# Performance work log

Hardware: AMD Instinct MI355X
Metric: run time of the kernel (lower is better)

The kernel has to match this reference:

```python
import jax, jax.numpy as jnp
import numpy as np


def setup_inputs() -> dict:
    key = jax.random.key(0)
    k1, k2, k3, k4 = jax.random.split(key, 4)
    B, Tv, Ta, D = 8, 2048, 2048, 256
    return {
        "visual_features": jax.random.normal(k1, (B, Tv, D), dtype=jnp.float32),
        "audio_features": jax.random.normal(k2, (B, Ta, D), dtype=jnp.float32),
        "visual_weights": jax.random.uniform(k3, (D, D), dtype=jnp.float32),
        "audio_weights": jax.random.uniform(k4, (D, D), dtype=jnp.float32),
        "num_neighbors": 8,
    }


def _pairwise_l2(vm, am):
    # ||v - a|| via the expanded form to avoid the [B,Tv,Ta,D] intermediate.
    sq = (
        jnp.sum(vm * vm, -1)[:, :, None]
        + jnp.sum(am * am, -1)[:, None, :]
        - 2.0 * jnp.einsum("btd,bsd->bts", vm, am)
    )
    sq = jnp.maximum(sq, 0.0)
    # safe sqrt: subgradient 0 at 0 (matches torch.norm backward convention)
    return jnp.where(sq > 0, jnp.sqrt(jnp.where(sq > 0, sq, 1.0)), 0.0)


def reference(visual_features, audio_features, visual_weights, audio_weights, num_neighbors):
    vm = visual_features @ visual_weights  # [B,Tv,D]
    am = audio_features @ audio_weights    # [B,Ta,D]
    graph = jnp.exp(-_pairwise_l2(vm, am))  # [B,Tv,Ta]
    # topk over the visual axis (dim=1): move it last for lax.top_k
    _, idx = jax.lax.top_k(jnp.swapaxes(graph, 1, 2), num_neighbors)  # [B,Ta,k]
    idx = jnp.swapaxes(idx, 1, 2)  # [B,k,Ta]
    # broadcasted gather along axis 1: result [B,k,Ta,D]
    vn = jnp.take_along_axis(visual_features[:, :, None, :], idx[..., None], axis=1)
    an = jnp.take_along_axis(audio_features[:, :, None, :], idx[..., None], axis=1)
    # mean over dim=2 (the Ta axis of the gathered neighbors) -> [B,k,D]
    return vn.mean(axis=2), an.mean(axis=2)
```

## Files before the change

### kernel.cpp

```cpp
#include <hip/hip_runtime.h>
#include <cstddef>
#include <cstdint>

namespace {
constexpr int kB   = 8;
constexpr int kT   = 2048;
constexpr int kD   = 256;
constexpr int kK   = 8;
constexpr int kM   = kB * kT;
constexpr int kNCH = 64;
constexpr int kNC  = kB * kT;
constexpr int kColCap = 64;
constexpr int kOvCap  = 1 << 17;
constexpr float kMinNormalF = 1.17549435e-38f;
}

typedef __attribute__((ext_vector_type(8)))  __bf16 bf16x8;
typedef __attribute__((ext_vector_type(16))) float  f32x16;

__device__ inline unsigned short f2bf_rne(float x) {
  unsigned u = __float_as_uint(x);
  unsigned r = (u + 0x7FFFu + ((u >> 16) & 1u)) >> 16;
  return (unsigned short)r;
}
__device__ inline float bf2f(unsigned short h) {
  return __uint_as_float((unsigned)h << 16);
}

__global__ __launch_bounds__(256) void transposeW2(const float* __restrict__ W0,
                                                   const float* __restrict__ W1,
                                                   unsigned short* __restrict__ T0,
                                                   unsigned short* __restrict__ T1) {
  const float* W = blockIdx.z ? W1 : W0;
  unsigned short* WT = blockIdx.z ? T1 : T0;
  __shared__ float tile[32][33];
  const int k0 = blockIdx.y * 32, c0 = blockIdx.x * 32;
  const int tx = threadIdx.x & 31, ty = threadIdx.x >> 5;
#pragma unroll
  for (int i = 0; i < 4; ++i)
    tile[ty + i * 8][tx] = W[(size_t)(k0 + ty + i * 8) * kD + c0 + tx];
  __syncthreads();
#pragma unroll
  for (int i = 0; i < 4; ++i)
    WT[(size_t)(c0 + ty + i * 8) * kD + k0 + tx] = f2bf_rne(tile[tx][ty + i * 8]);
}

__global__ __launch_bounds__(256) void gemm_fused(const float* __restrict__ Xv,
                                                  const float* __restrict__ Xa,
                                                  const unsigned short* __restrict__ WvT,
                                                  const unsigned short* __restrict__ WaT,
                                                  unsigned short* __restrict__ Cv,
                                                  unsigned short* __restrict__ Ca,
                                                  float* __restrict__ nv,
                                                  float* __restrict__ na) {
  __shared__ unsigned short Xs[128 * 68];
  __shared__ unsigned short Ws[64 * 68];
  const int z = blockIdx.z;
  const float* X = z ? Xa : Xv;
  const unsigned short* WT = z ? WaT : WvT;
  unsigned short* Cb = z ? Ca : Cv;
  float* nrm = z ? na : nv;
  const int r0 = blockIdx.x * 128;
  const int c0 = blockIdx.y * 64;
  const int tid = threadIdx.x;
  const int w = tid >> 6, lane = tid & 63;
  const int half = lane >> 5, ln = lane & 31;
  const int xrb = tid >> 4, xc4 = (tid & 15) * 4;
  const int wrb = tid >> 3, wc8 = (tid & 7) * 8;

  f32x16 acc[2];
#pragma unroll
  for (int j = 0; j < 2; ++j)
#pragma unroll
    for (int i = 0; i < 16; ++i) acc[j][i] = 0.0f;

  union Frag { uint2 u2[2]; bf16x8 v; };

  for (int k0 = 0; k0 < kD; k0 += 64) {
#pragma unroll
    for (int i = 0; i < 8; ++i) {
      const float4 v = *reinterpret_cast<const float4*>(X + (size_t)(r0 + i * 16 + xrb) * kD + k0 + xc4);
      ushort4 o;
      o.x = f2bf_rne(v.x); o.y = f2bf_rne(v.y); o.z = f2bf_rne(v.z); o.w = f2bf_rne(v.w);
      *reinterpret_cast<ushort4*>(Xs + (i * 16 + xrb) * 68 + xc4) = o;
    }
#pragma unroll
    for (int i = 0; i < 2; ++i) {
      const uint4 v = *reinterpret_cast<const uint4*>(WT + (size_t)(c0 + i * 32 + wrb) * kD + k0 + wc8);
      *reinterpret_cast<uint4*>(Ws + (i * 32 + wrb) * 68 + wc8) = v;
    }
    __syncthreads();
#pragma unroll
    for (int kk = 0; kk < 4; ++kk) {
      Frag fa, fb0, fb1;
      const uint2* pa = reinterpret_cast<const uint2*>(Xs + (w * 32 + ln) * 68 + kk * 16 + half * 8);
      fa.u2[0] = pa[0]; fa.u2[1] = pa[1];
      const uint2* p0 = reinterpret_cast<const uint2*>(Ws + ln * 68 + kk * 16 + half * 8);
      fb0.u2[0] = p0[0]; fb0.u2[1] = p0[1];
      const uint2* p1 = reinterpret_cast<const uint2*>(Ws + (32 + ln) * 68 + kk * 16 + half * 8);
      fb1.u2[0] = p1[0]; fb1.u2[1] = p1[1];
      acc[0] = __builtin_amdgcn_mfma_f32_32x32x16_bf16(fa.v, fb0.v, acc[0], 0, 0, 0);
      acc[1] = __builtin_amdgcn_mfma_f32_32x32x16_bf16(fa.v, fb1.v, acc[1], 0, 0, 0);
    }
    __syncthreads();
  }
  float ns[16];
#pragma unroll
  for (int r = 0; r < 16; ++r) ns[r] = 0.0f;
#pragma unroll
  for (int jj = 0; jj < 2; ++jj) {
    const int col = c0 + jj * 32 + ln;
#pragma unroll
    for (int r = 0; r < 16; ++r) {
      const int row = r0 + w * 32 + (r & 3) + 8 * (r >> 2) + 4 * half;
      const unsigned short us = f2bf_rne(acc[jj][r]);
      Cb[(size_t)row * kD + col] = us;
      const float f = bf2f(us);
      ns[r] += f * f;
    }
  }
#pragma unroll
  for (int r = 0; r < 16; ++r) {
    float v = ns[r];
#pragma unroll
    for (int off = 1; off < 32; off <<= 1) v += __shfl_xor(v, off, 64);
    if (ln == 0) {
      const int row = r0 + w * 32 + (r & 3) + 8 * (r >> 2) + 4 * half;
      atomicAdd(nrm + row, v);
    }
  }
}

__global__ __launch_bounds__(256) void keys_mfma(const unsigned short* __restrict__ vmb,
                                                 const unsigned short* __restrict__ amb,
                                                 const float* __restrict__ vn2,
                                                 const float* __restrict__ an2,
                                                 unsigned* __restrict__ colCount,
                                                 uint2* __restrict__ colRecs,
                                                 unsigned* __restrict__ ovCount,
                                                 uint2* __restrict__ ovRecs) {
  __shared__ unsigned short vmS[64 * 68];
  __shared__ unsigned short amS[64 * 68];
  const int b = blockIdx.z;
  const int t0 = blockIdx.x * 64;
  const int s0 = blockIdx.y * 64;
  const int tid = threadIdx.x;
  const int wave = tid >> 6, lane = tid & 63;
  const int wt = wave & 1, wsi = wave >> 1;
  const int half = lane >> 5, ln = lane & 31;
  const int rb = tid >> 3, c8 = (tid & 7) * 8;
  const unsigned short* vbase = vmb + ((size_t)b * kT + t0) * kD;
  const unsigned short* abase = amb + ((size_t)b * kT + s0) * kD;

  f32x16 acc;
#pragma unroll
  for (int i = 0; i < 16; ++i) acc[i] = 0.0f;

  union Frag { uint2 u2[2]; bf16x8 v; };

  for (int k0 = 0; k0 < kD; k0 += 64) {
#pragma unroll
    for (int i = 0; i < 2; ++i) {
      const int row = i * 32 + rb;
      const uint4 v = *reinterpret_cast<const uint4*>(vbase + (size_t)row * kD + k0 + c8);
      *reinterpret_cast<uint4*>(vmS + row * 68 + c8) = v;
      const uint4 a = *reinterpret_cast<const uint4*>(abase + (size_t)row * kD + k0 + c8);
      *reinterpret_cast<uint4*>(amS + row * 68 + c8) = a;
    }
    __syncthreads();
#pragma unroll
    for (int kk = 0; kk < 4; ++kk) {
      Frag fa, fb;
      const uint2* pa = reinterpret_cast<const uint2*>(vmS + (wt * 32 + ln) * 68 + kk * 16 + half * 8);
      fa.u2[0] = pa[0]; fa.u2[1] = pa[1];
      const uint2* pb = reinterpret_cast<const uint2*>(amS + (wsi * 32 + ln) * 68 + kk * 16 + half * 8);
      fb.u2[0] = pb[0]; fb.u2[1] = pb[1];
      acc = __builtin_amdgcn_mfma_f32_32x32x16_bf16(fa.v, fb.v, acc, 0, 0, 0);
    }
    __syncthreads();
  }

  const int s = s0 + wsi * 32 + ln;
  const float a2 = an2[(size_t)b * kT + s];
  const int c = (b << 11) | s;
  const float* v2p = vn2 + (size_t)b * kT + t0 + wt * 32;
#pragma unroll
  for (int g = 0; g < 4; ++g) {
    const float4 v2 = *reinterpret_cast<const float4*>(v2p + g * 8 + half * 4);
    const float v2a[4] = {v2.x, v2.y, v2.z, v2.w};
#pragma unroll
    for (int q = 0; q < 4; ++q) {
      const float dot = acc[4 * g + q];
      const float sq = fmaxf(v2a[q] + a2 - 2.0f * dot, 0.0f);
      const float dist = sqrtf(sq);
      if (dist < 88.0f) {
        const float e = expf(-dist);
        if (e >= kMinNormalF) {
          const int t = t0 + wt * 32 + g * 8 + half * 4 + q;
          const unsigned slot = atomicAdd(&colCount[c], 1u);
          if (slot < (unsigned)kColCap) {
            colRecs[(size_t)c * kColCap + slot] = make_uint2(__float_as_uint(e), (unsigned)t);
          } else {
            const unsigned pos = ((unsigned)b << 22) | ((unsigned)s << 11) | (unsigned)t;
            const unsigned oi = atomicAdd(ovCount, 1u);
            if (oi < (unsigned)kOvCap) ovRecs[oi] = make_uint2(__float_as_uint(e), pos);
          }
        }
      }
    }
  }
}

__global__ __launch_bounds__(256) void finalize_topk(const unsigned* __restrict__ colCount,
                                                     const uint2* __restrict__ colRecs,
                                                     const unsigned* __restrict__ ovCount,
                                                     const uint2* __restrict__ ovRecs,
                                                     int* __restrict__ idxT) {
  const int c = blockIdx.x * 256 + threadIdx.x;
  unsigned K[8];
  int T[8];
#pragma unroll
  for (int i = 0; i < 8; ++i) { K[i] = 0u; T[i] = 0x7FFFFFFF; }
  const int cnt = (int)colCount[c];
  const int m = min(cnt, kColCap);
  for (int i = 0; i < m; ++i) {
    const uint2 r = colRecs[(size_t)c * kColCap + i];
    const unsigned kx = r.x;
    const int tx = (int)r.y;
    if (kx > K[7] || (kx == K[7] && tx < T[7])) {
      K[7] = kx; T[7] = tx;
#pragma unroll
      for (int q = 7; q >= 1; --q) {
        const bool sw = (K[q] > K[q - 1]) || (K[q] == K[q - 1] && T[q] < T[q - 1]);
        if (sw) {
          const unsigned tk = K[q]; K[q] = K[q - 1]; K[q - 1] = tk;
          const int tt = T[q];      T[q] = T[q - 1]; T[q - 1] = tt;
        }
      }
    }
  }
  if (cnt > kColCap) {
    int n = (int)*ovCount;
    if (n > kOvCap) n = kOvCap;
    for (int i = 0; i < n; ++i) {
      const uint2 r = ovRecs[i];
      if ((int)(r.y >> 11) == c) {
        const unsigned kx = r.x;
        const int tx = (int)(r.y & 2047u);
        if (kx > K[7] || (kx == K[7] && tx < T[7])) {
          K[7] = kx; T[7] = tx;
#pragma unroll
          for (int q = 7; q >= 1; --q) {
            const bool sw = (K[q] > K[q - 1]) || (K[q] == K[q - 1] && T[q] < T[q - 1]);
            if (sw) {
              const unsigned tk = K[q]; K[q] = K[q - 1]; K[q - 1] = tk;
              const int tt = T[q];      T[q] = T[q - 1]; T[q - 1] = tt;
            }
          }
        }
      }
    }
  }
  int mcnt = 0;
#pragma unroll
  for (int i = 0; i < 8; ++i) if (K[i] > 0u) mcnt++;
  int outv[8];
#pragma unroll
  for (int i = 0; i < 8; ++i) outv[i] = T[i];
  int cand = 0;
  for (int r = mcnt; r < 8; ++r) {
    bool taken = true;
    while (taken) {
      taken = false;
#pragma unroll
      for (int q = 0; q < 8; ++q)
        if (q < mcnt && T[q] == cand) taken = true;
      if (taken) cand++;
    }
    outv[r] = cand++;
  }
  const int b = c >> 11, s = c & 2047;
#pragma unroll
  for (int r = 0; r < 8; ++r) idxT[((size_t)b * kK + r) * kT + s] = outv[r];
}

__global__ __launch_bounds__(256) void gather_kernel(const float* __restrict__ visual,
                                                     const float* __restrict__ audio,
                                                     const int* __restrict__ idxT,
                                                     float* __restrict__ pv,
                                                     float* __restrict__ pa) {
  const int blk = blockIdx.x;
  const int ch = blk & (kNCH - 1);
  const int bj = blk / kNCH;
  const int b = bj >> 3;
  const int d = threadIdx.x;
  const int* ip = idxT + (size_t)bj * kT + ch * (kT / kNCH);
  float accV = 0.f, accA = 0.f;
  for (int g = 0; g < kT / kNCH / 4; ++g) {
    const int4 cur = *reinterpret_cast<const int4*>(ip + g * 4);
    const int ts[4] = {cur.x, cur.y, cur.z, cur.w};
#pragma unroll
    for (int u = 0; u < 4; ++u) {
      const size_t base = ((size_t)b * kT + ts[u]) * kD + d;
      accV += visual[base];
      accA += audio[base];
    }
  }
  pv[(size_t)blk * kD + d] = accV;
  pa[(size_t)blk * kD + d] = accA;
}

__global__ __launch_bounds__(256) void reduce_kernel(const float* __restrict__ pv,
                                                     const float* __restrict__ pa,
                                                     float* __restrict__ out) {
  const int bj = blockIdx.x;
  const int d = threadIdx.x;
  float sV = 0.f, sA = 0.f;
#pragma unroll 8
  for (int ch = 0; ch < kNCH; ++ch) {
    sV += pv[((size_t)bj * kNCH + ch) * kD + d];
    sA += pa[((size_t)bj * kNCH + ch) * kD + d];
  }
  out[(size_t)bj * kD + d] = sV * (1.0f / kT);
  out[(size_t)kB * kK * kD + (size_t)bj * kD + d] = sA * (1.0f / kT);
}

extern "C" void kernel_launch(void* const* d_in, const int* in_sizes, int n_in,
                              void* d_out, int out_size, void* d_ws, size_t ws_size,
                              hipStream_t stream) {
  (void)in_sizes; (void)n_in; (void)out_size; (void)ws_size;
  const float* visual = (const float*)d_in[0];
  const float* audio  = (const float*)d_in[1];
  const float* Wv     = (const float*)d_in[2];
  const float* Wa     = (const float*)d_in[3];
  float* out = (float*)d_out;

  char* ws = (char*)d_ws;
  unsigned short* WvT = (unsigned short*)ws;
  unsigned short* WaT = WvT + (size_t)kD * kD;
  unsigned short* vmb = WaT + (size_t)kD * kD;
  unsigned short* amb = vmb + (size_t)kM * kD;
  float* vn2 = (float*)(amb + (size_t)kM * kD);
  float* an2 = vn2 + kM;
  unsigned* colCount = (unsigned*)(an2 + kM);
  unsigned* ovCount  = colCount + kNC;
  uint2* colRecs = (uint2*)(ovCount + 4);
  uint2* ovRecs  = colRecs + (size_t)kNC * kColCap;
  int* idxT = (int*)(ovRecs + kOvCap);
  float* pv = (float*)(idxT + (size_t)kB * kK * kT);
  float* pa = pv + (size_t)kB * kK * kNCH * kD;

  hipMemsetAsync(vn2, 0, (size_t)(2 * kM + kNC + 4) * sizeof(float), stream);
  transposeW2<<<dim3(kD / 32, kD / 32, 2), 256, 0, stream>>>(Wv, Wa, WvT, WaT);
  gemm_fused<<<dim3(kM / 128, kD / 64, 2), 256, 0, stream>>>(visual, audio, WvT, WaT,
                                                             vmb, amb, vn2, an2);
  keys_mfma<<<dim3(kT / 64, kT / 64, kB), 256, 0, stream>>>(vmb, amb, vn2, an2,
                                                            colCount, colRecs, ovCount, ovRecs);
  finalize_topk<<<dim3(kNC / 256), 256, 0, stream>>>(colCount, colRecs, ovCount, ovRecs, idxT);
  gather_kernel<<<dim3(kB * kK * kNCH), 256, 0, stream>>>(visual, audio, idxT, pv, pa);
  reduce_kernel<<<dim3(kB * kK), 256, 0, stream>>>(pv, pa, out);
}
```

Measured before the change: 175.5 us.

## Enlarge keys GEMM tile, reshape projection tile, fold reduce into gather atomics

The pairwise-distance MFMA kernel now computes a 64x128 tile per block, two MFMA accumulators per wave, so each loaded visual tile is reused across more audio columns and the block count halves. Its distance test now compares the squared distance against 7744 before taking the sqrt. The projection GEMM switches from a 128x64 to a 64x128 tile with a 2x2 wave layout. The separate reduce kernel is removed: gather blocks atomically add their scaled partial sums into a zeroed output, which saves a launch and the partial buffers but makes float summation order nondeterministic.

```diff
diff --git a/kernel.cpp b/kernel.cpp
--- a/kernel.cpp
+++ b/kernel.cpp
@@ -53,20 +53,19 @@
                                                   unsigned short* __restrict__ Ca,
                                                   float* __restrict__ nv,
                                                   float* __restrict__ na) {
-  __shared__ unsigned short Xs[128 * 68];
-  __shared__ unsigned short Ws[64 * 68];
+  __shared__ unsigned short Xs[64 * 68];
+  __shared__ unsigned short Ws[128 * 68];
   const int z = blockIdx.z;
   const float* X = z ? Xa : Xv;
   const unsigned short* WT = z ? WaT : WvT;
   unsigned short* Cb = z ? Ca : Cv;
   float* nrm = z ? na : nv;
-  const int r0 = blockIdx.x * 128;
-  const int c0 = blockIdx.y * 64;
+  const int r0 = blockIdx.x * 64;
+  const int c0 = blockIdx.y * 128;
   const int tid = threadIdx.x;
-  const int w = tid >> 6, lane = tid & 63;
+  const int wave = tid >> 6, lane = tid & 63;
+  const int wt = wave & 1, wsi = wave >> 1;
   const int half = lane >> 5, ln = lane & 31;
-  const int xrb = tid >> 4, xc4 = (tid & 15) * 4;
-  const int wrb = tid >> 3, wc8 = (tid & 7) * 8;
 
   f32x16 acc[2];
 #pragma unroll
@@ -78,26 +77,30 @@
 
   for (int k0 = 0; k0 < kD; k0 += 64) {
 #pragma unroll
-    for (int i = 0; i < 8; ++i) {
-      const float4 v = *reinterpret_cast<const float4*>(X + (size_t)(r0 + i * 16 + xrb) * kD + k0 + xc4);
+    for (int i = 0; i < 4; ++i) {
+      const int j = i * 256 + tid;
+      const int row = j >> 4, c4 = (j & 15) * 4;
+      const float4 v = *reinterpret_cast<const float4*>(X + (size_t)(r0 + row) * kD + k0 + c4);
       ushort4 o;
       o.x = f2bf_rne(v.x); o.y = f2bf_rne(v.y); o.z = f2bf_rne(v.z); o.w = f2bf_rne(v.w);
-      *reinterpret_cast<ushort4*>(Xs + (i * 16 + xrb) * 68 + xc4) = o;
-    }
-#pragma unroll
-    for (int i = 0; i < 2; ++i) {
-      const uint4 v = *reinterpret_cast<const uint4*>(WT + (size_t)(c0 + i * 32 + wrb) * kD + k0 + wc8);
-      *reinterpret_cast<uint4*>(Ws + (i * 32 + wrb) * 68 + wc8) = v;
+      *reinterpret_cast<ushort4*>(Xs + row * 68 + c4) = o;
+    }
+#pragma unroll
+    for (int i = 0; i < 4; ++i) {
+      const int j = i * 256 + tid;
+      const int row = j >> 3, c8 = (j & 7) * 8;
+      const uint4 v = *reinterpret_cast<const uint4*>(WT + (size_t)(c0 + row) * kD + k0 + c8);
+      *reinterpret_cast<uint4*>(Ws + row * 68 + c8) = v;
     }
     __syncthreads();
 #pragma unroll
     for (int kk = 0; kk < 4; ++kk) {
       Frag fa, fb0, fb1;
-      const uint2* pa = reinterpret_cast<const uint2*>(Xs + (w * 32 + ln) * 68 + kk * 16 + half * 8);
+      const uint2* pa = reinterpret_cast<const uint2*>(Xs + (wt * 32 + ln) * 68 + kk * 16 + half * 8);
       fa.u2[0] = pa[0]; fa.u2[1] = pa[1];
-      const uint2* p0 = reinterpret_cast<const uint2*>(Ws + ln * 68 + kk * 16 + half * 8);
+      const uint2* p0 = reinterpret_cast<const uint2*>(Ws + (wsi * 64 + ln) * 68 + kk * 16 + half * 8);
       fb0.u2[0] = p0[0]; fb0.u2[1] = p0[1];
-      const uint2* p1 = reinterpret_cast<const uint2*>(Ws + (32 + ln) * 68 + kk * 16 + half * 8);
+      const uint2* p1 = reinterpret_cast<const uint2*>(Ws + (wsi * 64 + 32 + ln) * 68 + kk * 16 + half * 8);
       fb1.u2[0] = p1[0]; fb1.u2[1] = p1[1];
       acc[0] = __builtin_amdgcn_mfma_f32_32x32x16_bf16(fa.v, fb0.v, acc[0], 0, 0, 0);
       acc[1] = __builtin_amdgcn_mfma_f32_32x32x16_bf16(fa.v, fb1.v, acc[1], 0, 0, 0);
@@ -109,10 +112,10 @@
   for (int r = 0; r < 16; ++r) ns[r] = 0.0f;
 #pragma unroll
   for (int jj = 0; jj < 2; ++jj) {
-    const int col = c0 + jj * 32 + ln;
+    const int col = c0 + wsi * 64 + jj * 32 + ln;
 #pragma unroll
     for (int r = 0; r < 16; ++r) {
-      const int row = r0 + w * 32 + (r & 3) + 8 * (r >> 2) + 4 * half;
+      const int row = r0 + wt * 32 + (r & 3) + 8 * (r >> 2) + 4 * half;
       const unsigned short us = f2bf_rne(acc[jj][r]);
       Cb[(size_t)row * kD + col] = us;
       const float f = bf2f(us);
@@ -125,7 +128,7 @@
 #pragma unroll
     for (int off = 1; off < 32; off <<= 1) v += __shfl_xor(v, off, 64);
     if (ln == 0) {
-      const int row = r0 + w * 32 + (r & 3) + 8 * (r >> 2) + 4 * half;
+      const int row = r0 + wt * 32 + (r & 3) + 8 * (r >> 2) + 4 * half;
       atomicAdd(nrm + row, v);
     }
   }
@@ -140,70 +143,82 @@
                                                  unsigned* __restrict__ ovCount,
                                                  uint2* __restrict__ ovRecs) {
   __shared__ unsigned short vmS[64 * 68];
-  __shared__ unsigned short amS[64 * 68];
+  __shared__ unsigned short amS[128 * 68];
   const int b = blockIdx.z;
   const int t0 = blockIdx.x * 64;
-  const int s0 = blockIdx.y * 64;
+  const int s0 = blockIdx.y * 128;
   const int tid = threadIdx.x;
   const int wave = tid >> 6, lane = tid & 63;
   const int wt = wave & 1, wsi = wave >> 1;
   const int half = lane >> 5, ln = lane & 31;
-  const int rb = tid >> 3, c8 = (tid & 7) * 8;
   const unsigned short* vbase = vmb + ((size_t)b * kT + t0) * kD;
   const unsigned short* abase = amb + ((size_t)b * kT + s0) * kD;
 
-  f32x16 acc;
-#pragma unroll
-  for (int i = 0; i < 16; ++i) acc[i] = 0.0f;
+  f32x16 acc[2];
+#pragma unroll
+  for (int j = 0; j < 2; ++j)
+#pragma unroll
+    for (int i = 0; i < 16; ++i) acc[j][i] = 0.0f;
 
   union Frag { uint2 u2[2]; bf16x8 v; };
 
   for (int k0 = 0; k0 < kD; k0 += 64) {
 #pragma unroll
     for (int i = 0; i < 2; ++i) {
-      const int row = i * 32 + rb;
+      const int j = i * 256 + tid;
+      const int row = j >> 3, c8 = (j & 7) * 8;
       const uint4 v = *reinterpret_cast<const uint4*>(vbase + (size_t)row * kD + k0 + c8);
       *reinterpret_cast<uint4*>(vmS + row * 68 + c8) = v;
+    }
+#pragma unroll
+    for (int i = 0; i < 4; ++i) {
+      const int j = i * 256 + tid;
+      const int row = j >> 3, c8 = (j & 7) * 8;
       const uint4 a = *reinterpret_cast<const uint4*>(abase + (size_t)row * kD + k0 + c8);
       *reinterpret_cast<uint4*>(amS + row * 68 + c8) = a;
     }
     __syncthreads();
 #pragma unroll
     for (int kk = 0; kk < 4; ++kk) {
-      Frag fa, fb;
+      Frag fa, fb0, fb1;
       const uint2* pa = reinterpret_cast<const uint2*>(vmS + (wt * 32 + ln) * 68 + kk * 16 + half * 8);
       fa.u2[0] = pa[0]; fa.u2[1] = pa[1];
-      const uint2* pb = reinterpret_cast<const uint2*>(amS + (wsi * 32 + ln) * 68 + kk * 16 + half * 8);
-      fb.u2[0] = pb[0]; fb.u2[1] = pb[1];
-      acc = __builtin_amdgcn_mfma_f32_32x32x16_bf16(fa.v, fb.v, acc, 0, 0, 0);
+      const uint2* p0 = reinterpret_cast<const uint2*>(amS + (wsi * 64 + ln) * 68 + kk * 16 + half * 8);
+      fb0.u2[0] = p0[0]; fb0.u2[1] = p0[1];
+      const uint2* p1 = reinterpret_cast<const uint2*>(amS + (wsi * 64 + 32 + ln) * 68 + kk * 16 + half * 8);
+      fb1.u2[0] = p1[0]; fb1.u2[1] = p1[1];
+      acc[0] = __builtin_amdgcn_mfma_f32_32x32x16_bf16(fa.v, fb0.v, acc[0], 0, 0, 0);
+      acc[1] = __builtin_amdgcn_mfma_f32_32x32x16_bf16(fa.v, fb1.v, acc[1], 0, 0, 0);
     }
     __syncthreads();
   }
 
-  const int s = s0 + wsi * 32 + ln;
-  const float a2 = an2[(size_t)b * kT + s];
-  const int c = (b << 11) | s;
   const float* v2p = vn2 + (size_t)b * kT + t0 + wt * 32;
 #pragma unroll
-  for (int g = 0; g < 4; ++g) {
-    const float4 v2 = *reinterpret_cast<const float4*>(v2p + g * 8 + half * 4);
-    const float v2a[4] = {v2.x, v2.y, v2.z, v2.w};
-#pragma unroll
-    for (int q = 0; q < 4; ++q) {
-      const float dot = acc[4 * g + q];
-      const float sq = fmaxf(v2a[q] + a2 - 2.0f * dot, 0.0f);
-      const float dist = sqrtf(sq);
-      if (dist < 88.0f) {
-        const float e = expf(-dist);
-        if (e >= kMinNormalF) {
-          const int t = t0 + wt * 32 + g * 8 + half * 4 + q;
-          const unsigned slot = atomicAdd(&colCount[c], 1u);
-          if (slot < (unsigned)kColCap) {
-            colRecs[(size_t)c * kColCap + slot] = make_uint2(__float_as_uint(e), (unsigned)t);
-          } else {
-            const unsigned pos = ((unsigned)b << 22) | ((unsigned)s << 11) | (unsigned)t;
-            const unsigned oi = atomicAdd(ovCount, 1u);
-            if (oi < (unsigned)kOvCap) ovRecs[oi] = make_uint2(__float_as_uint(e), pos);
+  for (int j = 0; j < 2; ++j) {
+    const int s = s0 + wsi * 64 + j * 32 + ln;
+    const float a2 = an2[(size_t)b * kT + s];
+    const int c = (b << 11) | s;
+#pragma unroll
+    for (int g = 0; g < 4; ++g) {
+      const float4 v2 = *reinterpret_cast<const float4*>(v2p + g * 8 + half * 4);
+      const float v2a[4] = {v2.x, v2.y, v2.z, v2.w};
+#pragma unroll
+      for (int q = 0; q < 4; ++q) {
+        const float raw = v2a[q] + a2 - 2.0f * acc[j][4 * g + q];
+        if (raw < 7744.0f) {
+          const float dist = sqrtf(fmaxf(raw, 0.0f));
+          const float e = expf(-dist);
+          if (e >= kMinNormalF) {
+            const int t = t0 + wt * 32 + g * 8 + half * 4 + q;
+            const unsigned slot = atomicAdd(&colCount[c], 1u);
+            if (slot < (unsigned)kColCap) {
+              colRecs[(size_t)c * kColCap + slot] = make_uint2(__float_as_uint(e), (unsigned)t);
+            } else {
+              const unsigned pos = ((unsigned)b << 22) | ((unsigned)s << 11) | (unsigned)t;
+              const unsigned oi = atomicAdd(ovCount, 1u);
+              if (oi < (unsigned)kOvCap) ovRecs[oi] = make_uint2(__float_as_uint(e), pos);
+            }
           }
         }
       }
@@ -287,8 +302,7 @@
 __global__ __launch_bounds__(256) void gather_kernel(const float* __restrict__ visual,
                                                      const float* __restrict__ audio,
                                                      const int* __restrict__ idxT,
-                                                     float* __restrict__ pv,
-                                                     float* __restrict__ pa) {
+                                                     float* __restrict__ out) {
   const int blk = blockIdx.x;
   const int ch = blk & (kNCH - 1);
   const int bj = blk / kNCH;
@@ -306,29 +320,14 @@
       accA += audio[base];
     }
   }
-  pv[(size_t)blk * kD + d] = accV;
-  pa[(size_t)blk * kD + d] = accA;
-}
-
-__global__ __launch_bounds__(256) void reduce_kernel(const float* __restrict__ pv,
-                                                     const float* __restrict__ pa,
-                                                     float* __restrict__ out) {
-  const int bj = blockIdx.x;
-  const int d = threadIdx.x;
-  float sV = 0.f, sA = 0.f;
-#pragma unroll 8
-  for (int ch = 0; ch < kNCH; ++ch) {
-    sV += pv[((size_t)bj * kNCH + ch) * kD + d];
-    sA += pa[((size_t)bj * kNCH + ch) * kD + d];
-  }
-  out[(size_t)bj * kD + d] = sV * (1.0f / kT);
-  out[(size_t)kB * kK * kD + (size_t)bj * kD + d] = sA * (1.0f / kT);
+  atomicAdd(out + (size_t)bj * kD + d, accV * (1.0f / kT));
+  atomicAdd(out + (size_t)kB * kK * kD + (size_t)bj * kD + d, accA * (1.0f / kT));
 }
 
 extern "C" void kernel_launch(void* const* d_in, const int* in_sizes, int n_in,
                               void* d_out, int out_size, void* d_ws, size_t ws_size,
                               hipStream_t stream) {
-  (void)in_sizes; (void)n_in; (void)out_size; (void)ws_size;
+  (void)in_sizes; (void)n_in; (void)ws_size;
   const float* visual = (const float*)d_in[0];
   const float* audio  = (const float*)d_in[1];
   const float* Wv     = (const float*)d_in[2];
@@ -347,16 +346,14 @@
   uint2* colRecs = (uint2*)(ovCount + 4);
   uint2* ovRecs  = colRecs + (size_t)kNC * kColCap;
   int* idxT = (int*)(ovRecs + kOvCap);
-  float* pv = (float*)(idxT + (size_t)kB * kK * kT);
-  float* pa = pv + (size_t)kB * kK * kNCH * kD;
-
+
+  hipMemsetAsync(out, 0, (size_t)out_size * sizeof(float), stream);
   hipMemsetAsync(vn2, 0, (size_t)(2 * kM + kNC + 4) * sizeof(float), stream);
   transposeW2<<<dim3(kD / 32, kD / 32, 2), 256, 0, stream>>>(Wv, Wa, WvT, WaT);
-  gemm_fused<<<dim3(kM / 128, kD / 64, 2), 256, 0, stream>>>(visual, audio, WvT, WaT,
+  gemm_fused<<<dim3(kM / 64, kD / 128, 2), 256, 0, stream>>>(visual, audio, WvT, WaT,
                                                              vmb, amb, vn2, an2);
-  keys_mfma<<<dim3(kT / 64, kT / 64, kB), 256, 0, stream>>>(vmb, amb, vn2, an2,
-                                                            colCount, colRecs, ovCount, ovRecs);
+  keys_mfma<<<dim3(kT / 64, kT / 128, kB), 256, 0, stream>>>(vmb, amb, vn2, an2,
+                                                             colCount, colRecs, ovCount, ovRecs);
   finalize_topk<<<dim3(kNC / 256), 256, 0, stream>>>(colCount, colRecs, ovCount, ovRecs, idxT);
-  gather_kernel<<<dim3(kB * kK * kNCH), 256, 0, stream>>>(visual, audio, idxT, pv, pa);
-  reduce_kernel<<<dim3(kB * kK), 256, 0, stream>>>(pv, pa, out);
-}
+  gather_kernel<<<dim3(kB * kK * kNCH), 256, 0, stream>>>(visual, audio, idxT, out);
+}
```

Result: no change. 178.6 us (+1.8%).

## Keep A fragments in registers and enlarge pairwise tile to 128x128

Applied to the files above, without the earlier changes.

Both the projection GEMM and the pairwise-distance GEMM now load each wave's A-operand rows (full K=256) straight into registers as bf16 fragments, and stage only the B operand in LDS for the full K depth with a padded stride. This removes the per-K-chunk barrier loop. The distance kernel's tile grows from 64x64 to 128x128 and loops over two 64-wide audio subtiles, so each visual row is reused more. The distance threshold check is done on the squared value before the sqrt. In exchange, register pressure rises (16 uint4 A fragments per thread) and LDS use per block grows, which may reduce occupancy.

```diff
diff --git a/kernel.cpp b/kernel.cpp
--- a/kernel.cpp
+++ b/kernel.cpp
@@ -12,6 +12,7 @@
 constexpr int kNC  = kB * kT;
 constexpr int kColCap = 64;
 constexpr int kOvCap  = 1 << 17;
+constexpr int kStr = 264;
 constexpr float kMinNormalF = 1.17549435e-38f;
 }
 
@@ -26,6 +27,7 @@
 __device__ inline float bf2f(unsigned short h) {
   return __uint_as_float((unsigned)h << 16);
 }
+union FragU { uint4 u4; bf16x8 v; };
 
 __global__ __launch_bounds__(256) void transposeW2(const float* __restrict__ W0,
                                                    const float* __restrict__ W1,
@@ -45,16 +47,15 @@
     WT[(size_t)(c0 + ty + i * 8) * kD + k0 + tx] = f2bf_rne(tile[tx][ty + i * 8]);
 }
 
-__global__ __launch_bounds__(256) void gemm_fused(const float* __restrict__ Xv,
-                                                  const float* __restrict__ Xa,
-                                                  const unsigned short* __restrict__ WvT,
-                                                  const unsigned short* __restrict__ WaT,
-                                                  unsigned short* __restrict__ Cv,
-                                                  unsigned short* __restrict__ Ca,
-                                                  float* __restrict__ nv,
-                                                  float* __restrict__ na) {
-  __shared__ unsigned short Xs[128 * 68];
-  __shared__ unsigned short Ws[64 * 68];
+__global__ __launch_bounds__(256) void gemm_areg(const float* __restrict__ Xv,
+                                                 const float* __restrict__ Xa,
+                                                 const unsigned short* __restrict__ WvT,
+                                                 const unsigned short* __restrict__ WaT,
+                                                 unsigned short* __restrict__ Cv,
+                                                 unsigned short* __restrict__ Ca,
+                                                 float* __restrict__ nv,
+                                                 float* __restrict__ na) {
+  __shared__ unsigned short Ws[64 * kStr];
   const int z = blockIdx.z;
   const float* X = z ? Xa : Xv;
   const unsigned short* WT = z ? WaT : WvT;
@@ -65,55 +66,51 @@
   const int tid = threadIdx.x;
   const int w = tid >> 6, lane = tid & 63;
   const int half = lane >> 5, ln = lane & 31;
-  const int xrb = tid >> 4, xc4 = (tid & 15) * 4;
-  const int wrb = tid >> 3, wc8 = (tid & 7) * 8;
-
+
+#pragma unroll
+  for (int i = 0; i < 8; ++i) {
+    const int idx = i * 256 + tid;
+    const int row = idx >> 5, g = idx & 31;
+    const uint4 v = *reinterpret_cast<const uint4*>(WT + (size_t)(c0 + row) * kD + g * 8);
+    *reinterpret_cast<uint4*>(Ws + row * kStr + g * 8) = v;
+  }
+  const float* xrow = X + (size_t)(r0 + w * 32 + ln) * kD + half * 8;
+  uint4 afr[16];
+#pragma unroll
+  for (int kc = 0; kc < 16; ++kc) {
+    const float4 v0 = *reinterpret_cast<const float4*>(xrow + kc * 16);
+    const float4 v1 = *reinterpret_cast<const float4*>(xrow + kc * 16 + 4);
+    afr[kc].x = (unsigned)f2bf_rne(v0.x) | ((unsigned)f2bf_rne(v0.y) << 16);
+    afr[kc].y = (unsigned)f2bf_rne(v0.z) | ((unsigned)f2bf_rne(v0.w) << 16);
+    afr[kc].z = (unsigned)f2bf_rne(v1.x) | ((unsigned)f2bf_rne(v1.y) << 16);
+    afr[kc].w = (unsigned)f2bf_rne(v1.z) | ((unsigned)f2bf_rne(v1.w) << 16);
+  }
   f32x16 acc[2];
 #pragma unroll
   for (int j = 0; j < 2; ++j)
 #pragma unroll
     for (int i = 0; i < 16; ++i) acc[j][i] = 0.0f;
-
-  union Frag { uint2 u2[2]; bf16x8 v; };
-
-  for (int k0 = 0; k0 < kD; k0 += 64) {
-#pragma unroll
-    for (int i = 0; i < 8; ++i) {
-      const float4 v = *reinterpret_cast<const float4*>(X + (size_t)(r0 + i * 16 + xrb) * kD + k0 + xc4);
-      ushort4 o;
-      o.x = f2bf_rne(v.x); o.y = f2bf_rne(v.y); o.z = f2bf_rne(v.z); o.w = f2bf_rne(v.w);
-      *reinterpret_cast<ushort4*>(Xs + (i * 16 + xrb) * 68 + xc4) = o;
-    }
-#pragma unroll
-    for (int i = 0; i < 2; ++i) {
-      const uint4 v = *reinterpret_cast<const uint4*>(WT + (size_t)(c0 + i * 32 + wrb) * kD + k0 + wc8);
-      *reinterpret_cast<uint4*>(Ws + (i * 32 + wrb) * 68 + wc8) = v;
-    }
-    __syncthreads();
-#pragma unroll
-    for (int kk = 0; kk < 4; ++kk) {
-      Frag fa, fb0, fb1;
-      const uint2* pa = reinterpret_cast<const uint2*>(Xs + (w * 32 + ln) * 68 + kk * 16 + half * 8);
-      fa.u2[0] = pa[0]; fa.u2[1] = pa[1];
-      const uint2* p0 = reinterpret_cast<const uint2*>(Ws + ln * 68 + kk * 16 + half * 8);
-      fb0.u2[0] = p0[0]; fb0.u2[1] = p0[1];
-      const uint2* p1 = reinterpret_cast<const uint2*>(Ws + (32 + ln) * 68 + kk * 16 + half * 8);
-      fb1.u2[0] = p1[0]; fb1.u2[1] = p1[1];
-      acc[0] = __builtin_amdgcn_mfma_f32_32x32x16_bf16(fa.v, fb0.v, acc[0], 0, 0, 0);
-      acc[1] = __builtin_amdgcn_mfma_f32_32x32x16_bf16(fa.v, fb1.v, acc[1], 0, 0, 0);
-    }
-    __syncthreads();
+  __syncthreads();
+#pragma unroll
+  for (int kc = 0; kc < 16; ++kc) {
+    FragU fa; fa.u4 = afr[kc];
+#pragma unroll
+    for (int cs = 0; cs < 2; ++cs) {
+      FragU fb;
+      fb.u4 = *reinterpret_cast<const uint4*>(Ws + (cs * 32 + ln) * kStr + kc * 16 + half * 8);
+      acc[cs] = __builtin_amdgcn_mfma_f32_32x32x16_bf16(fa.v, fb.v, acc[cs], 0, 0, 0);
+    }
   }
   float ns[16];
 #pragma unroll
   for (int r = 0; r < 16; ++r) ns[r] = 0.0f;
 #pragma unroll
-  for (int jj = 0; jj < 2; ++jj) {
-    const int col = c0 + jj * 32 + ln;
+  for (int cs = 0; cs < 2; ++cs) {
+    const int col = c0 + cs * 32 + ln;
 #pragma unroll
     for (int r = 0; r < 16; ++r) {
       const int row = r0 + w * 32 + (r & 3) + 8 * (r >> 2) + 4 * half;
-      const unsigned short us = f2bf_rne(acc[jj][r]);
+      const unsigned short us = f2bf_rne(acc[cs][r]);
       Cb[(size_t)row * kD + col] = us;
       const float f = bf2f(us);
       ns[r] += f * f;
@@ -131,7 +128,7 @@
   }
 }
 
-__global__ __launch_bounds__(256) void keys_mfma(const unsigned short* __restrict__ vmb,
+__global__ __launch_bounds__(256) void keys_areg(const unsigned short* __restrict__ vmb,
                                                  const unsigned short* __restrict__ amb,
                                                  const float* __restrict__ vn2,
                                                  const float* __restrict__ an2,
@@ -139,71 +136,74 @@
                                                  uint2* __restrict__ colRecs,
                                                  unsigned* __restrict__ ovCount,
                                                  uint2* __restrict__ ovRecs) {
-  __shared__ unsigned short vmS[64 * 68];
-  __shared__ unsigned short amS[64 * 68];
+  __shared__ unsigned short amS[64 * kStr];
   const int b = blockIdx.z;
-  const int t0 = blockIdx.x * 64;
-  const int s0 = blockIdx.y * 64;
+  const int t0 = blockIdx.x * 128;
+  const int sr0 = blockIdx.y * 128;
   const int tid = threadIdx.x;
-  const int wave = tid >> 6, lane = tid & 63;
-  const int wt = wave & 1, wsi = wave >> 1;
+  const int w = tid >> 6, lane = tid & 63;
   const int half = lane >> 5, ln = lane & 31;
-  const int rb = tid >> 3, c8 = (tid & 7) * 8;
-  const unsigned short* vbase = vmb + ((size_t)b * kT + t0) * kD;
-  const unsigned short* abase = amb + ((size_t)b * kT + s0) * kD;
-
-  f32x16 acc;
-#pragma unroll
-  for (int i = 0; i < 16; ++i) acc[i] = 0.0f;
-
-  union Frag { uint2 u2[2]; bf16x8 v; };
-
-  for (int k0 = 0; k0 < kD; k0 += 64) {
-#pragma unroll
-    for (int i = 0; i < 2; ++i) {
-      const int row = i * 32 + rb;
-      const uint4 v = *reinterpret_cast<const uint4*>(vbase + (size_t)row * kD + k0 + c8);
-      *reinterpret_cast<uint4*>(vmS + row * 68 + c8) = v;
-      const uint4 a = *reinterpret_cast<const uint4*>(abase + (size_t)row * kD + k0 + c8);
-      *reinterpret_cast<uint4*>(amS + row * 68 + c8) = a;
-    }
+
+  const unsigned short* arow = vmb + ((size_t)b * kT + t0 + w * 32 + ln) * kD + half * 8;
+  uint4 afr[16];
+#pragma unroll
+  for (int kc = 0; kc < 16; ++kc)
+    afr[kc] = *reinterpret_cast<const uint4*>(arow + kc * 16);
+
+  const float* v2p = vn2 + (size_t)b * kT + t0 + w * 32;
+
+  for (int st = 0; st < 2; ++st) {
+    const int s0 = sr0 + st * 64;
+    if (st) __syncthreads();
+#pragma unroll
+    for (int i = 0; i < 8; ++i) {
+      const int idx = i * 256 + tid;
+      const int row = idx >> 5, g = idx & 31;
+      const uint4 v = *reinterpret_cast<const uint4*>(amb + ((size_t)b * kT + s0 + row) * kD + g * 8);
+      *reinterpret_cast<uint4*>(amS + row * kStr + g * 8) = v;
+    }
+    f32x16 acc[2];
+#pragma unroll
+    for (int j = 0; j < 2; ++j)
+#pragma unroll
+      for (int i = 0; i < 16; ++i) acc[j][i] = 0.0f;
     __syncthreads();
 #pragma unroll
-    for (int kk = 0; kk < 4; ++kk) {
-      Frag fa, fb;
-      const uint2* pa = reinterpret_cast<const uint2*>(vmS + (wt * 32 + ln) * 68 + kk * 16 + half * 8);
-      fa.u2[0] = pa[0]; fa.u2[1] = pa[1];
-      const uint2* pb = reinterpret_cast<const uint2*>(amS + (wsi * 32 + ln) * 68 + kk * 16 + half * 8);
-      fb.u2[0] = pb[0]; fb.u2[1] = pb[1];
-      acc = __builtin_amdgcn_mfma_f32_32x32x16_bf16(fa.v, fb.v, acc, 0, 0, 0);
-    }
-    __syncthreads();
-  }
-
-  const int s = s0 + wsi * 32 + ln;
-  const float a2 = an2[(size_t)b * kT + s];
-  const int c = (b << 11) | s;
-  const float* v2p = vn2 + (size_t)b * kT + t0 + wt * 32;
-#pragma unroll
-  for (int g = 0; g < 4; ++g) {
-    const float4 v2 = *reinterpret_cast<const float4*>(v2p + g * 8 + half * 4);
-    const float v2a[4] = {v2.x, v2.y, v2.z, v2.w};
-#pragma unroll
-    for (int q = 0; q < 4; ++q) {
-      const float dot = acc[4 * g + q];
-      const float sq = fmaxf(v2a[q] + a2 - 2.0f * dot, 0.0f);
-      const float dist = sqrtf(sq);
-      if (dist < 88.0f) {
-        const float e = expf(-dist);
-        if (e >= kMinNormalF) {
-          const int t = t0 + wt * 32 + g * 8 + half * 4 + q;
-          const unsigned slot = atomicAdd(&colCount[c], 1u);
-          if (slot < (unsigned)kColCap) {
-            colRecs[(size_t)c * kColCap + slot] = make_uint2(__float_as_uint(e), (unsigned)t);
-          } else {
-            const unsigned pos = ((unsigned)b << 22) | ((unsigned)s << 11) | (unsigned)t;
-            const unsigned oi = atomicAdd(ovCount, 1u);
-            if (oi < (unsigned)kOvCap) ovRecs[oi] = make_uint2(__float_as_uint(e), pos);
+    for (int kc = 0; kc < 16; ++kc) {
+      FragU fa; fa.u4 = afr[kc];
+#pragma unroll
+      for (int ss = 0; ss < 2; ++ss) {
+        FragU fb;
+        fb.u4 = *reinterpret_cast<const uint4*>(amS + (ss * 32 + ln) * kStr + kc * 16 + half * 8);
+        acc[ss] = __builtin_amdgcn_mfma_f32_32x32x16_bf16(fa.v, fb.v, acc[ss], 0, 0, 0);
+      }
+    }
+#pragma unroll
+    for (int ss = 0; ss < 2; ++ss) {
+      const int s = s0 + ss * 32 + ln;
+      const float a2 = an2[(size_t)b * kT + s];
+      const int c = (b << 11) | s;
+#pragma unroll
+      for (int g = 0; g < 4; ++g) {
+        const float4 v2 = *reinterpret_cast<const float4*>(v2p + g * 8 + half * 4);
+        const float v2a[4] = {v2.x, v2.y, v2.z, v2.w};
+#pragma unroll
+        for (int q = 0; q < 4; ++q) {
+          const float raw = v2a[q] + a2 - 2.0f * acc[ss][4 * g + q];
+          if (raw < 7744.0f) {
+            const float dist = sqrtf(fmaxf(raw, 0.0f));
+            const float e = expf(-dist);
+            if (e >= kMinNormalF) {
+              const int t = t0 + w * 32 + g * 8 + half * 4 + q;
+              const unsigned slot = atomicAdd(&colCount[c], 1u);
+              if (slot < (unsigned)kColCap) {
+                colRecs[(size_t)c * kColCap + slot] = make_uint2(__float_as_uint(e), (unsigned)t);
+              } else {
+                const unsigned pos = ((unsigned)b << 22) | ((unsigned)s << 11) | (unsigned)t;
+                const unsigned oi = atomicAdd(ovCount, 1u);
+                if (oi < (unsigned)kOvCap) ovRecs[oi] = make_uint2(__float_as_uint(e), pos);
+              }
+            }
           }
         }
       }
@@ -352,10 +352,10 @@
 
   hipMemsetAsync(vn2, 0, (size_t)(2 * kM + kNC + 4) * sizeof(float), stream);
   transposeW2<<<dim3(kD / 32, kD / 32, 2), 256, 0, stream>>>(Wv, Wa, WvT, WaT);
-  gemm_fused<<<dim3(kM / 128, kD / 64, 2), 256, 0, stream>>>(visual, audio, WvT, WaT,
-                                                             vmb, amb, vn2, an2);
-  keys_mfma<<<dim3(kT / 64, kT / 64, kB), 256, 0, stream>>>(vmb, amb, vn2, an2,
-                                                            colCount, colRecs, ovCount, ovRecs);
+  gemm_areg<<<dim3(kM / 128, kD / 64, 2), 256, 0, stream>>>(visual, audio, WvT, WaT,
+                                                            vmb, amb, vn2, an2);
+  keys_areg<<<dim3(kT / 128, kT / 128, kB), 256, 0, stream>>>(vmb, amb, vn2, an2,
+                                                              colCount, colRecs, ovCount, ovRecs);
   finalize_topk<<<dim3(kNC / 256), 256, 0, stream>>>(colCount, colRecs, ovCount, ovRecs, idxT);
   gather_kernel<<<dim3(kB * kK * kNCH), 256, 0, stream>>>(visual, audio, idxT, pv, pa);
   reduce_kernel<<<dim3(kB * kK), 256, 0, stream>>>(pv, pa, out);
```

Measured after the change: 173.8 us. Within noise of the previous version (-1.0%).
